# Optimization experiments

Hardware: AMD Instinct MI355X
Metric: run time of the kernel (lower is better)

The kernel has to match this reference:

```python
import jax, jax.numpy as jnp
import numpy as np

B, T = 8, 2048
IN, OUT = 1024, 1024
M, C = 32, 32
MIN_P, MAX_P = 1.0, 1024.0
EPS = 1e-5


def setup_inputs() -> dict:
    key = jax.random.key(0)
    ks = jax.random.split(key, 4)
    x = jax.random.normal(ks[0], (B, T, IN), dtype=jnp.float32)
    # pre: Linear(IN, 2*M + 2*OUT); mix: Linear(2*M*C, OUT)
    pre_w = jax.random.normal(ks[1], (IN, 2 * M + 2 * OUT), dtype=jnp.float32) / np.sqrt(IN)
    pre_b = jnp.zeros((2 * M + 2 * OUT,), jnp.float32)
    mix_w = jax.random.normal(ks[2], (2 * M * C, OUT), dtype=jnp.float32) / np.sqrt(2 * M * C)
    mix_b = jnp.zeros((OUT,), jnp.float32)
    # FFA decay/oscillation params (paper init): gamma_{m,c} = exp(-|a_m| + i b_c)
    a = jnp.linspace(1e-6, 0.5, M, dtype=jnp.float32)
    b = 2.0 * jnp.pi / jnp.linspace(MIN_P, MAX_P, C, dtype=jnp.float32)
    return dict(x=x, pre_w=pre_w, pre_b=pre_b, mix_w=mix_w, mix_b=mix_b, a=a, b=b)


def _ffa(u, a, b):
    """Complex-decay linear recurrence: s_t = gamma * s_{t-1} + u_t (s_0 = 0).

    u: [B,T,M] real input (broadcast over context dim C).
    Returns all states: [B,T,M,C] complex64.
    """
    log_gamma = (-jnp.abs(a))[:, None] + 1j * b[None, :]  # [M,C]
    gamma = jnp.exp(log_gamma).astype(jnp.complex64)
    Tn = u.shape[1]
    h = jnp.broadcast_to(u[..., None].astype(jnp.complex64), u.shape + (C,))  # [B,T,M,C]
    h = jnp.moveaxis(h, 1, 0)  # [T,B,M,C]
    p = jnp.broadcast_to(gamma, (Tn, 1, M, C))  # [T,1,M,C] time-invariant decay

    def combine(e1, e2):
        p1, h1 = e1
        p2, h2 = e2
        return (p1 * p2, h1 * p2 + h2)

    _, hs = jax.lax.associative_scan(combine, (p, h), axis=0)
    return jnp.moveaxis(hs, 0, 1)  # [B,T,M,C]


def reference(x, pre_w, pre_b, mix_w, mix_b, a, b):
    Bx, Tx, _ = x.shape
    pre = x @ pre_w + pre_b  # [B,T,2M+2OUT]
    y, thru, gate = jnp.split(pre, [M, M + OUT], axis=-1)
    gate = jax.nn.sigmoid(gate)
    in_gate, out_gate = gate[..., :M], gate[..., M:]
    s = _ffa(y * in_gate, a, b)  # [B,T,M,C] complex64
    # torch.view_as_real -> [...,M,C,2] then flatten -> interleaved (re,im)
    zr = jnp.stack([s.real, s.imag], axis=-1).reshape(Bx, Tx, 2 * M * C)
    z = zr @ mix_w + mix_b  # [B,T,OUT]
    # LayerNorm (no affine)
    z = (z - z.mean(-1, keepdims=True)) / jnp.sqrt(z.var(-1, keepdims=True) + EPS)
    out = z * out_gate + thru * (1.0 - out_gate)
    return out, s
```

## Files before the change

### kernel.cpp

```cpp
#include <hip/hip_runtime.h>
#include <stdint.h>

typedef __attribute__((ext_vector_type(2))) __bf16 bf16x2;
typedef __attribute__((ext_vector_type(4))) __bf16 bf16x4;
typedef __attribute__((ext_vector_type(8))) __bf16 bf16x8;
typedef __attribute__((ext_vector_type(4))) float f32x4;

#define DEV __device__ __forceinline__

DEV void g2lds16(const void* g, void* l) {
  __builtin_amdgcn_global_load_lds(
      (const __attribute__((address_space(1))) void*)g,
      (__attribute__((address_space(3))) void*)l, 16, 0, 0);
}

__global__ __launch_bounds__(256) void cvt_f32_bf16(const float* __restrict__ s,
                                                    __bf16* __restrict__ d, int n) {
  int i = (blockIdx.x * 256 + threadIdx.x) * 4;
  if (i >= n) return;
  float4 v = *reinterpret_cast<const float4*>(s + i);
  bf16x4 o;
  o[0] = (__bf16)v.x; o[1] = (__bf16)v.y; o[2] = (__bf16)v.z; o[3] = (__bf16)v.w;
  *reinterpret_cast<bf16x4*>(d + i) = o;
}

__global__ __launch_bounds__(256) void transpose_to_bf16(const float* __restrict__ src,
                                                         __bf16* __restrict__ dst,
                                                         int K, int N, int Npad) {
  __shared__ float tile[32][33];
  int n0 = blockIdx.x * 32, k0 = blockIdx.y * 32;
  int tx = threadIdx.x & 31, ty = threadIdx.x >> 5;
#pragma unroll
  for (int j = 0; j < 4; ++j) {
    int k = k0 + ty + j * 8;
    int n = n0 + tx;
    float v = 0.f;
    if (n < N) v = src[(long)k * N + n];
    tile[ty + j * 8][tx] = v;
  }
  __syncthreads();
#pragma unroll
  for (int j = 0; j < 4; ++j) {
    int n = n0 + ty + j * 8;
    int k = k0 + tx;
    if (n < Npad) dst[(long)n * K + k] = (__bf16)tile[tx][ty + j * 8];
  }
}

template <bool OUT_BF16>
__global__ __launch_bounds__(256) void gemm_mfma(const __bf16* __restrict__ A,
                                                 const __bf16* __restrict__ Wt,
                                                 const float* __restrict__ bias,
                                                 void* __restrict__ Cout,
                                                 int K, int Nreal, int ldc) {
  __shared__ __bf16 As[128 * 32];
  __shared__ __bf16 Bs[128 * 32];
  const int tid = threadIdx.x;
  const int lane = tid & 63, wid = tid >> 6;
  const int tm = blockIdx.y * 128, tn = blockIdx.x * 128;
  const int wr = (wid >> 1) * 64, wc = (wid & 1) * 64;

  f32x4 acc[4][4] = {};

  const int r0 = tid >> 2, c0 = (tid & 3) * 8;
  const int r1 = (tid + 256) >> 2, c1 = c0;

  int aoff[4], boff[4];
#pragma unroll
  for (int i = 0; i < 4; ++i) {
    aoff[i] = (wr + i * 16 + (lane & 15)) * 32 + (lane >> 4) * 8;
    boff[i] = (wc + i * 16 + (lane & 15)) * 32 + (lane >> 4) * 8;
  }

  const __bf16* Arow0 = A + (long)(tm + r0) * K + c0;
  const __bf16* Arow1 = A + (long)(tm + r1) * K + c1;
  const __bf16* Wrow0 = Wt + (long)(tn + r0) * K + c0;
  const __bf16* Wrow1 = Wt + (long)(tn + r1) * K + c1;

  for (int k0 = 0; k0 < K; k0 += 32) {
    g2lds16(Arow0 + k0, As + tid * 8);
    g2lds16(Arow1 + k0, As + (tid + 256) * 8);
    g2lds16(Wrow0 + k0, Bs + tid * 8);
    g2lds16(Wrow1 + k0, Bs + (tid + 256) * 8);
    __syncthreads();
    bf16x8 af[4], bw[4];
#pragma unroll
    for (int i = 0; i < 4; ++i) af[i] = *reinterpret_cast<const bf16x8*>(&As[aoff[i]]);
#pragma unroll
    for (int i = 0; i < 4; ++i) bw[i] = *reinterpret_cast<const bf16x8*>(&Bs[boff[i]]);
#pragma unroll
    for (int mi = 0; mi < 4; ++mi)
#pragma unroll
      for (int ni = 0; ni < 4; ++ni)
        acc[mi][ni] = __builtin_amdgcn_mfma_f32_16x16x32_bf16(af[mi], bw[ni],
                                                              acc[mi][ni], 0, 0, 0);
    __syncthreads();
  }

  const int rbase = tm + wr + ((lane >> 4) * 4);
  const int cbase = tn + wc + (lane & 15);
#pragma unroll
  for (int mi = 0; mi < 4; ++mi) {
#pragma unroll
    for (int ni = 0; ni < 4; ++ni) {
      int col = cbase + ni * 16;
      if (col < Nreal) {
        float bv = bias[col];
#pragma unroll
        for (int r = 0; r < 4; ++r) {
          long row = rbase + mi * 16 + r;
          float v = acc[mi][ni][r] + bv;
          if (OUT_BF16) ((__bf16*)Cout)[row * ldc + col] = (__bf16)v;
          else          ((float*)Cout)[row * ldc + col] = v;
        }
      }
    }
  }
}

__global__ __launch_bounds__(256) void u_kernel(const __bf16* __restrict__ pre,
                                                float* __restrict__ u) {
  int i = blockIdx.x * 8 + (threadIdx.x >> 5);
  int m = threadIdx.x & 31;
  const __bf16* pr = pre + (long)i * 2112;
  float y = (float)pr[m];
  float g = (float)pr[1056 + m];
  float sg = 1.f / (1.f + expf(-g));
  int b = i >> 11, t = i & 2047;
  u[(long)((b * 32) + m) * 2048 + t] = y * sg;
}

__global__ __launch_bounds__(64) void scan_kernel(const float* __restrict__ u,
                                                  const float* __restrict__ a,
                                                  const float* __restrict__ bfr,
                                                  __bf16* __restrict__ s_bf,
                                                  float* __restrict__ s_re) {
  int blk = blockIdx.x;
  int b = blk >> 4, mp = blk & 15;
  int lane = threadIdx.x;
  int mh = lane >> 5, c = lane & 31;
  int m = mp * 2 + mh;
  const float* ub = u + (long)(b * 32 + m) * 2048;
  float decay = expf(-fabsf(a[m]));
  float gr = decay * cosf(bfr[c]);
  float gi = decay * sinf(bfr[c]);
  float sr = 0.f, si = 0.f;
  long base = (long)b * 2048 * 1024 + m * 32 + c;
  for (int t = 0; t < 2048; ++t) {
    float uv = ub[t];
    float nr = fmaf(gr, sr, fmaf(-gi, si, uv));
    float ni_ = fmaf(gr, si, gi * sr);
    sr = nr; si = ni_;
    long ci = base + (long)t * 1024;
    bf16x2 zv; zv[0] = (__bf16)sr; zv[1] = (__bf16)si;
    *reinterpret_cast<bf16x2*>(s_bf + 2 * ci) = zv;
    s_re[ci] = sr;
  }
}

__global__ __launch_bounds__(64) void ln_plain(float* __restrict__ z,
                                               const __bf16* __restrict__ pre) {
  const long row = blockIdx.x;
  float* zp = z + row * 1024;
  const int tid = threadIdx.x;
  float v[16];
  float s = 0.f, ss = 0.f;
#pragma unroll
  for (int q = 0; q < 16; ++q) {
    float x = zp[tid + q * 64];
    v[q] = x; s += x; ss += x * x;
  }
#pragma unroll
  for (int o = 32; o > 0; o >>= 1) {
    s += __shfl_down(s, o, 64);
    ss += __shfl_down(ss, o, 64);
  }
  s = __shfl(s, 0, 64);
  ss = __shfl(ss, 0, 64);
  float mean = s * (1.f / 1024.f);
  float var = ss * (1.f / 1024.f) - mean * mean;
  float rstd = rsqrtf(var + 1e-5f);
  const __bf16* pr = pre + row * 2112;
#pragma unroll
  for (int q = 0; q < 16; ++q) {
    int e = tid + q * 64;
    float th = (float)pr[32 + e];
    float og = (float)pr[1088 + e];
    float g = 1.f / (1.f + expf(-og));
    zp[e] = (v[q] - mean) * rstd * g + th * (1.f - g);
  }
}

extern "C" void kernel_launch(void* const* d_in, const int* in_sizes, int n_in,
                              void* d_out, int out_size, void* d_ws, size_t ws_size,
                              hipStream_t stream) {
  const float* x = (const float*)d_in[0];
  const float* pre_w = (const float*)d_in[1];
  const float* pre_b = (const float*)d_in[2];
  const float* mix_w = (const float*)d_in[3];
  const float* mix_b = (const float*)d_in[4];
  const float* a = (const float*)d_in[5];
  const float* bfr = (const float*)d_in[6];

  char* ws = (char*)d_ws;
  __bf16* buf0  = (__bf16*)(ws + 0);
  __bf16* preWT = (__bf16*)(ws + 67108864);
  __bf16* mixWT = (__bf16*)(ws + 71565312);
  __bf16* pre   = (__bf16*)(ws + 75759616);
  float*  u     = (float*)(ws + 144965632);
  const size_t WS_NEEDED = 147062784ull;
  if (ws_size < WS_NEEDED) return;

  __bf16* x_bf = buf0;
  __bf16* s_bf = buf0;

  float* out0 = (float*)d_out;
  float* s_re = out0 + 16777216;

  cvt_f32_bf16<<<16384, 256, 0, stream>>>(x, x_bf, 16777216);
  transpose_to_bf16<<<dim3(68, 32), 256, 0, stream>>>(pre_w, preWT, 1024, 2112, 2176);
  transpose_to_bf16<<<dim3(32, 64), 256, 0, stream>>>(mix_w, mixWT, 2048, 1024, 1024);
  gemm_mfma<true><<<dim3(17, 128), 256, 0, stream>>>(x_bf, preWT, pre_b, pre,
                                                     1024, 2112, 2112);
  u_kernel<<<2048, 256, 0, stream>>>(pre, u);
  scan_kernel<<<128, 64, 0, stream>>>(u, a, bfr, s_bf, s_re);
  gemm_mfma<false><<<dim3(8, 128), 256, 0, stream>>>(s_bf, mixWT, mix_b, out0,
                                                     2048, 1024, 1024);
  ln_plain<<<16384, 64, 0, stream>>>(out0, pre);
}
```

Baseline: 384.1 us.

## Double-buffer LDS tiles in MFMA GEMM to overlap loads with compute

New measurement: 383.4 us. No clear change (-0.2%).

```diff
diff --git a/kernel.cpp b/kernel.cpp
--- a/kernel.cpp
+++ b/kernel.cpp
@@ -53,8 +53,8 @@
                                                  const float* __restrict__ bias,
                                                  void* __restrict__ Cout,
                                                  int K, int Nreal, int ldc) {
-  __shared__ __bf16 As[128 * 32];
-  __shared__ __bf16 Bs[128 * 32];
+  __shared__ __bf16 As[2][128 * 32];
+  __shared__ __bf16 Bs[2][128 * 32];
   const int tid = threadIdx.x;
   const int lane = tid & 63, wid = tid >> 6;
   const int tm = blockIdx.y * 128, tn = blockIdx.x * 128;
@@ -63,7 +63,7 @@
   f32x4 acc[4][4] = {};
 
   const int r0 = tid >> 2, c0 = (tid & 3) * 8;
-  const int r1 = (tid + 256) >> 2, c1 = c0;
+  const int r1 = r0 + 64;
 
   int aoff[4], boff[4];
 #pragma unroll
@@ -73,21 +73,30 @@
   }
 
   const __bf16* Arow0 = A + (long)(tm + r0) * K + c0;
-  const __bf16* Arow1 = A + (long)(tm + r1) * K + c1;
+  const __bf16* Arow1 = A + (long)(tm + r1) * K + c0;
   const __bf16* Wrow0 = Wt + (long)(tn + r0) * K + c0;
-  const __bf16* Wrow1 = Wt + (long)(tn + r1) * K + c1;
-
-  for (int k0 = 0; k0 < K; k0 += 32) {
-    g2lds16(Arow0 + k0, As + tid * 8);
-    g2lds16(Arow1 + k0, As + (tid + 256) * 8);
-    g2lds16(Wrow0 + k0, Bs + tid * 8);
-    g2lds16(Wrow1 + k0, Bs + (tid + 256) * 8);
-    __syncthreads();
+  const __bf16* Wrow1 = Wt + (long)(tn + r1) * K + c0;
+
+  g2lds16(Arow0, As[0] + tid * 8);
+  g2lds16(Arow1, As[0] + (tid + 256) * 8);
+  g2lds16(Wrow0, Bs[0] + tid * 8);
+  g2lds16(Wrow1, Bs[0] + (tid + 256) * 8);
+  __syncthreads();
+
+  const int nt = K >> 5;
+  int cur = 0;
+  for (int t = 1; t < nt; ++t) {
+    const int k0 = t << 5;
+    const int nxt = cur ^ 1;
+    g2lds16(Arow0 + k0, As[nxt] + tid * 8);
+    g2lds16(Arow1 + k0, As[nxt] + (tid + 256) * 8);
+    g2lds16(Wrow0 + k0, Bs[nxt] + tid * 8);
+    g2lds16(Wrow1 + k0, Bs[nxt] + (tid + 256) * 8);
     bf16x8 af[4], bw[4];
 #pragma unroll
-    for (int i = 0; i < 4; ++i) af[i] = *reinterpret_cast<const bf16x8*>(&As[aoff[i]]);
-#pragma unroll
-    for (int i = 0; i < 4; ++i) bw[i] = *reinterpret_cast<const bf16x8*>(&Bs[boff[i]]);
+    for (int i = 0; i < 4; ++i) af[i] = *reinterpret_cast<const bf16x8*>(&As[cur][aoff[i]]);
+#pragma unroll
+    for (int i = 0; i < 4; ++i) bw[i] = *reinterpret_cast<const bf16x8*>(&Bs[cur][boff[i]]);
 #pragma unroll
     for (int mi = 0; mi < 4; ++mi)
 #pragma unroll
@@ -95,6 +104,20 @@
         acc[mi][ni] = __builtin_amdgcn_mfma_f32_16x16x32_bf16(af[mi], bw[ni],
                                                               acc[mi][ni], 0, 0, 0);
     __syncthreads();
+    cur = nxt;
+  }
+  {
+    bf16x8 af[4], bw[4];
+#pragma unroll
+    for (int i = 0; i < 4; ++i) af[i] = *reinterpret_cast<const bf16x8*>(&As[cur][aoff[i]]);
+#pragma unroll
+    for (int i = 0; i < 4; ++i) bw[i] = *reinterpret_cast<const bf16x8*>(&Bs[cur][boff[i]]);
+#pragma unroll
+    for (int mi = 0; mi < 4; ++mi)
+#pragma unroll
+      for (int ni = 0; ni < 4; ++ni)
+        acc[mi][ni] = __builtin_amdgcn_mfma_f32_16x16x32_bf16(af[mi], bw[ni],
+                                                              acc[mi][ni], 0, 0, 0);
   }
 
   const int rbase = tm + wr + ((lane >> 4) * 4);
```
